# Kernel tuning notes

Hardware: AMD Instinct MI355X
Metric: run time of the kernel (lower is better)

## Reference

```python
import jax, jax.numpy as jnp
import numpy as np

N_HEADS = 8
N_LEVELS = 1
N_POINTS = 4
D_MODEL = 256
BATCH = 2
H0, W0 = 100, 150
LS = H0 * W0
LQ = 15000


def layer_norm(x, g, b, eps=1e-5):
    m = jnp.mean(x, -1, keepdims=True)
    v = jnp.var(x, -1, keepdims=True)
    return (x - m) * jax.lax.rsqrt(v + eps) * g + b


def bilinear_sample(v, Hl, Wl, loc):
    # v: [N, Hl*Wl, Hh, D] level features; loc in [0,1]: [N, Lq, Hh, P, 2] (x, y)
    Nb, _, Hh, D = v.shape
    Lq, P = loc.shape[1], loc.shape[3]
    x = loc[..., 0] * Wl - 0.5           # align_corners=False grid_sample convention
    y = loc[..., 1] * Hl - 0.5
    x0 = jnp.floor(x); y0 = jnp.floor(y)
    lx = (x - x0).transpose(0, 2, 1, 3)[..., None]   # [N,Hh,Lq,P,1]
    ly = (y - y0).transpose(0, 2, 1, 3)[..., None]
    x0i = x0.astype(jnp.int32); y0i = y0.astype(jnp.int32)
    vh = v.transpose(0, 2, 1, 3)                      # [N,Hh,Hl*Wl,D]

    def gather(xi, yi):
        valid = (xi >= 0) & (xi < Wl) & (yi >= 0) & (yi < Hl)   # zero padding
        idx = jnp.clip(yi, 0, Hl - 1) * Wl + jnp.clip(xi, 0, Wl - 1)
        idxf = idx.transpose(0, 2, 1, 3).reshape(Nb, Hh, Lq * P)
        g = jnp.take_along_axis(vh, idxf[..., None], axis=2).reshape(Nb, Hh, Lq, P, D)
        return g * valid.transpose(0, 2, 1, 3)[..., None]

    g00 = gather(x0i, y0i)
    g10 = gather(x0i + 1, y0i)
    g01 = gather(x0i, y0i + 1)
    g11 = gather(x0i + 1, y0i + 1)
    return (g00 * (1 - lx) * (1 - ly) + g10 * lx * (1 - ly)
            + g01 * (1 - lx) * ly + g11 * lx * ly)   # [N,Hh,Lq,P,D]


def ms_deform_attn(q, reference_points, src, shapes_np, starts_np, padding_mask,
                   W_val, b_val, W_off, b_off, W_attn, b_attn, W_out, b_out):
    Nb, Lq, C = q.shape
    Hh, D, L, P = N_HEADS, C // N_HEADS, N_LEVELS, N_POINTS
    value = src @ W_val + b_val
    value = jnp.where(padding_mask[..., None], 0.0, value).reshape(Nb, -1, Hh, D)
    offsets = (q @ W_off + b_off).reshape(Nb, Lq, Hh, L, P, 2)
    aw = jax.nn.softmax((q @ W_attn + b_attn).reshape(Nb, Lq, Hh, L * P), -1)
    aw = aw.reshape(Nb, Lq, Hh, L, P)
    # offset normalizer is (W, H) per level
    norm = jnp.asarray(shapes_np[:, ::-1].copy(), dtype=q.dtype)   # [L,2]
    loc = reference_points[:, :, None, :, None, :] + offsets / norm[None, None, None, :, None, :]
    out = 0.0
    for l in range(L):
        Hl, Wl = int(shapes_np[l, 0]), int(shapes_np[l, 1])
        s = int(starts_np[l])
        sampled = bilinear_sample(value[:, s:s + Hl * Wl], Hl, Wl, loc[:, :, :, l])
        out = out + jnp.sum(sampled * aw[:, :, :, l].transpose(0, 2, 1, 3)[..., None], axis=3)
    out = out.transpose(0, 2, 1, 3).reshape(Nb, Lq, C)
    return out @ W_out + b_out


def reference(tgt, query_pos, src_pos, tgt_spatial_shapes, reference_points,
              depth_reference_points, src, src_spatial_shapes, frame_start_index,
              src_padding_mask,
              W_dsa, b_dsa, g_nds, b_nds, W_off, b_off, W_attn, b_attn,
              W_val, b_val, W_out, b_out, W_csa, b_csa, g_n1, b_n1,
              W_ff, b_ff, g_n3, b_n3):
    ss = np.asarray(src_spatial_shapes)      # static level shapes
    starts = np.asarray(frame_start_index)
    # depth scale adaptation
    src_a = layer_norm(src @ W_dsa + b_dsa, g_nds, b_nds)
    q = tgt + query_pos
    tgt2 = ms_deform_attn(q, reference_points, src_a, ss, starts, src_padding_mask,
                          W_val, b_val, W_off, b_off, W_attn, b_attn, W_out, b_out)
    tgt2 = tgt2 @ W_csa + b_csa
    t = layer_norm(tgt + tgt2, g_n1, b_n1)
    # FFN: single linear d_model->d_model with exact GELU (per source code)
    ff = jax.nn.gelu(t @ W_ff + b_ff, approximate=False)
    return layer_norm(t + ff, g_n3, b_n3)


def setup_inputs() -> dict:
    key = jax.random.key(0)
    ks = jax.random.split(key, 24)
    C = D_MODEL
    Hh, L, P = N_HEADS, N_LEVELS, N_POINTS

    def lin(k, fin, fout, scale=None):
        s = (1.0 / np.sqrt(fin)) if scale is None else scale
        return (jax.random.normal(k, (fin, fout), jnp.float32) * s).astype(jnp.float32)

    inp = {}
    inp['tgt'] = jax.random.normal(ks[0], (BATCH, LQ, C), jnp.float32)
    inp['query_pos'] = 0.1 * jax.random.normal(ks[1], (BATCH, LQ, C), jnp.float32)
    inp['src_pos'] = 0.1 * jax.random.normal(ks[2], (BATCH, LS, C), jnp.float32)
    inp['tgt_spatial_shapes'] = jnp.array([[H0, W0]], jnp.int32)
    inp['reference_points'] = jax.random.uniform(ks[3], (BATCH, LQ, L, 2), jnp.float32)
    inp['depth_reference_points'] = jax.random.uniform(ks[4], (BATCH, LQ, 1, 2), jnp.float32)
    inp['src'] = jax.random.normal(ks[5], (BATCH, LS, C), jnp.float32)
    inp['src_spatial_shapes'] = jnp.array([[H0, W0]], jnp.int32)
    inp['frame_start_index'] = jnp.array([0], jnp.int32)
    inp['src_padding_mask'] = jnp.zeros((BATCH, LS), jnp.bool_)
    # parameters
    inp['W_dsa'] = lin(ks[6], C, C); inp['b_dsa'] = jnp.zeros((C,), jnp.float32)
    inp['g_nds'] = jnp.ones((C,), jnp.float32); inp['b_nds'] = jnp.zeros((C,), jnp.float32)
    inp['W_off'] = lin(ks[7], C, Hh * L * P * 2, scale=0.01)
    inp['b_off'] = 0.5 * jax.random.normal(ks[8], (Hh * L * P * 2,), jnp.float32)
    inp['W_attn'] = lin(ks[9], C, Hh * L * P)
    inp['b_attn'] = jnp.zeros((Hh * L * P,), jnp.float32)
    inp['W_val'] = lin(ks[10], C, C); inp['b_val'] = jnp.zeros((C,), jnp.float32)
    inp['W_out'] = lin(ks[11], C, C); inp['b_out'] = jnp.zeros((C,), jnp.float32)
    inp['W_csa'] = lin(ks[12], C, C); inp['b_csa'] = jnp.zeros((C,), jnp.float32)
    inp['g_n1'] = jnp.ones((C,), jnp.float32); inp['b_n1'] = jnp.zeros((C,), jnp.float32)
    inp['W_ff'] = lin(ks[13], C, C); inp['b_ff'] = jnp.zeros((C,), jnp.float32)
    inp['g_n3'] = jnp.ones((C,), jnp.float32); inp['b_n3'] = jnp.zeros((C,), jnp.float32)
    return inp
```

## Files before the change

### kernel.cpp

```cpp
#include <hip/hip_runtime.h>
#include <hip/hip_bf16.h>
#include <math.h>

#define LQ   15000
#define LS_  15000
#define NB   2
#define ROWS (NB*LQ)
#define HGT  100
#define WID  150

typedef __attribute__((ext_vector_type(8))) short bf16x8;
typedef __attribute__((ext_vector_type(4))) float f32x4;

__device__ inline short f2bf(float x) {
    __hip_bfloat16 h = __float2bfloat16(x);
    return *reinterpret_cast<short*>(&h);
}
__device__ inline unsigned pack2bf(float a, float b) {
    return ((unsigned)(unsigned short)f2bf(a)) | (((unsigned)(unsigned short)f2bf(b)) << 16);
}
__device__ inline float bf2f(short s) {
    return __uint_as_float(((unsigned)(unsigned short)s) << 16);
}
__device__ inline float gelu_exact(float x) {
    return 0.5f * x * (1.f + erff(x * 0.70710678118654752440f));
}

#if defined(__has_builtin)
#if __has_builtin(__builtin_amdgcn_global_load_lds)
#define HAS_GLL 1
#endif
#endif
#ifndef HAS_GLL
#define HAS_GLL 0
#endif

typedef unsigned int u32;

__device__ __forceinline__ void gld_lds16(const void* g, void* l) {
#if HAS_GLL
    __builtin_amdgcn_global_load_lds(
        (const __attribute__((address_space(1))) u32*)g,
        (__attribute__((address_space(3))) u32*)l,
        16, 0, 0);
#else
    int lane = threadIdx.x & 63;
    *(int4*)((char*)l + lane * 16) = *(const int4*)g;
#endif
}

template<int MODE>
__global__ __launch_bounds__(256, 2) void fused2(
    const void* __restrict__ Ap,
    const short* __restrict__ W1T, const float* __restrict__ bias1,
    const float* __restrict__ res1,
    const float* __restrict__ g1v, const float* __restrict__ b1v,
    const short* __restrict__ W2T, const float* __restrict__ bias2,
    void* __restrict__ Out,
    const unsigned char* __restrict__ mask,
    const float* __restrict__ g2v, const float* __restrict__ b2v,
    int M)
{
    __shared__ __align__(16) char lds[2 * 16384 + 64 * 264 * 2];
    short (*T)[264] = (short(*)[264])(lds + 32768);

    const int tid = threadIdx.x;
    const int bm0 = blockIdx.x * 64;
    const int wave = tid >> 6, lane = tid & 63;
    const int quad = lane >> 4, c = lane & 15;

    const int roff = c * 64 + ((quad ^ ((c >> 1) & 3)) << 4);

    auto stageB = [&](int buf, const short* __restrict__ W, int k0) {
        #pragma unroll
        for (int it = 0; it < 4; ++it) {
            int s = it * 256 + wave * 64 + lane;
            int n = s >> 2;
            int j = (s & 3) ^ ((n >> 1) & 3);
            gld_lds16(W + (size_t)n * 256 + k0 + j * 8,
                      lds + buf * 16384 + (it * 256 + wave * 64) * 16);
        }
    };

    int rA = bm0 + wave * 16 + c; if (rA > M - 1) rA = M - 1;
    bf16x8 aReg[8];

    stageB(0, W1T, 0);

    if (MODE == 1) {
        const short* A = (const short*)Ap + (size_t)rA * 256 + quad * 8;
        #pragma unroll
        for (int k = 0; k < 8; ++k) aReg[k] = *(const bf16x8*)(A + k * 32);
    } else {
        const float* A = (const float*)Ap + (size_t)rA * 256 + quad * 8;
        float4 lo[8], hi[8];
        #pragma unroll
        for (int k = 0; k < 8; ++k) {
            lo[k] = *(const float4*)(A + k * 32);
            hi[k] = *(const float4*)(A + k * 32 + 4);
        }
        #pragma unroll
        for (int k = 0; k < 8; ++k) {
            union { int4 i; bf16x8 v; } u;
            u.i.x = pack2bf(lo[k].x, lo[k].y);
            u.i.y = pack2bf(lo[k].z, lo[k].w);
            u.i.z = pack2bf(hi[k].x, hi[k].y);
            u.i.w = pack2bf(hi[k].z, hi[k].w);
            aReg[k] = u.v;
        }
    }

    f32x4 acc[16];
    #pragma unroll
    for (int t = 0; t < 16; ++t) acc[t] = (f32x4){0.f, 0.f, 0.f, 0.f};

    __syncthreads();

    #pragma unroll
    for (int k0c = 0; k0c < 8; ++k0c) {
        if (k0c < 7) stageB((k0c + 1) & 1, W1T, (k0c + 1) * 32);
        const char* bb = lds + (k0c & 1) * 16384 + roff;
        bf16x8 a = aReg[k0c];
        #pragma unroll
        for (int t = 0; t < 16; ++t) {
            bf16x8 b = *(const bf16x8*)(bb + t * 1024);
            acc[t] = __builtin_amdgcn_mfma_f32_16x16x32_bf16(a, b, acc[t], 0, 0, 0);
        }
        __syncthreads();
    }

    stageB(0, W2T, 0);

    {
        const int rb = wave * 16 + quad * 4;
        #pragma unroll
        for (int reg = 0; reg < 4; ++reg) {
            int rloc = rb + reg;
            int rg = bm0 + rloc; int rgl = (rg < M) ? rg : (M - 1);
            float s = 0.f, sq = 0.f;
            float vv[16];
            #pragma unroll
            for (int t = 0; t < 16; ++t) {
                int col = t * 16 + c;
                float v = acc[t][reg] + bias1[col];
                if (MODE == 1) v += res1[(size_t)rgl * 256 + col];
                vv[t] = v; s += v; sq += v * v;
            }
            #pragma unroll
            for (int o = 1; o < 16; o <<= 1) {
                s += __shfl_xor(s, o, 64); sq += __shfl_xor(sq, o, 64);
            }
            float mean = s * (1.f / 256.f);
            float var  = sq * (1.f / 256.f) - mean * mean;
            float rs   = rsqrtf(var + 1e-5f);
            #pragma unroll
            for (int t = 0; t < 16; ++t) {
                int col = t * 16 + c;
                T[rloc][col] = f2bf((vv[t] - mean) * rs * g1v[col] + b1v[col]);
            }
        }
    }

    #pragma unroll
    for (int k = 0; k < 8; ++k)
        aReg[k] = *(const bf16x8*)&T[wave * 16 + c][k * 32 + quad * 8];

    #pragma unroll
    for (int t = 0; t < 16; ++t) acc[t] = (f32x4){0.f, 0.f, 0.f, 0.f};

    __syncthreads();

    #pragma unroll
    for (int k0c = 0; k0c < 8; ++k0c) {
        if (k0c < 7) stageB((k0c + 1) & 1, W2T, (k0c + 1) * 32);
        const char* bb = lds + (k0c & 1) * 16384 + roff;
        bf16x8 a = aReg[k0c];
        #pragma unroll
        for (int t = 0; t < 16; ++t) {
            bf16x8 b = *(const bf16x8*)(bb + t * 1024);
            acc[t] = __builtin_amdgcn_mfma_f32_16x16x32_bf16(a, b, acc[t], 0, 0, 0);
        }
        __syncthreads();
    }

    const int rb = wave * 16 + quad * 4;
    if constexpr (MODE == 0) {
        short* O = (short*)Out;
        #pragma unroll
        for (int reg = 0; reg < 4; ++reg) {
            int rloc = rb + reg; int r = bm0 + rloc;
            if (r < M) {
                float mz = mask[r] ? 0.f : 1.f;
                int n = (r >= LS_) ? 1 : 0;
                int sidx = r - n * LS_;
                #pragma unroll
                for (int t = 0; t < 16; ++t) {
                    int col = t * 16 + c; int h = col >> 5, d = col & 31;
                    O[(((size_t)n * 8 + h) * LS_ + sidx) * 32 + d] =
                        f2bf((acc[t][reg] + bias2[col]) * mz);
                }
            }
        }
    } else {
        float* O = (float*)Out;
        #pragma unroll
        for (int reg = 0; reg < 4; ++reg) {
            int rloc = rb + reg; int r = bm0 + rloc;
            float s = 0.f, sq = 0.f;
            float vv[16];
            #pragma unroll
            for (int t = 0; t < 16; ++t) {
                int col = t * 16 + c;
                float v = gelu_exact(acc[t][reg] + bias2[col]) + bf2f(T[rloc][col]);
                vv[t] = v; s += v; sq += v * v;
            }
            #pragma unroll
            for (int o = 1; o < 16; o <<= 1) {
                s += __shfl_xor(s, o, 64); sq += __shfl_xor(sq, o, 64);
            }
            float mean = s * (1.f / 256.f);
            float var  = sq * (1.f / 256.f) - mean * mean;
            float rs   = rsqrtf(var + 1e-5f);
            if (r < M) {
                #pragma unroll
                for (int t = 0; t < 16; ++t) {
                    int col = t * 16 + c;
                    O[(size_t)r * 256 + col] = (vv[t] - mean) * rs * g2v[col] + b2v[col];
                }
            }
        }
    }
}

__global__ __launch_bounds__(256) void oa_gemm(
    const float* __restrict__ tgt, const float* __restrict__ qpos,
    const short* __restrict__ WToa, const float* __restrict__ b_oa,
    float* __restrict__ S_oa, int M)
{
    __shared__ short As[64][40];
    __shared__ short Bs[96][40];
    __shared__ float sb[96];

    const int tid = threadIdx.x;
    const int bm0 = blockIdx.x * 64;
    const int wave = tid >> 6, lane = tid & 63;
    const int quad = lane >> 4, c = lane & 15;

    if (tid < 96) sb[tid] = b_oa[tid];

    f32x4 acc[6];
    #pragma unroll
    for (int t = 0; t < 6; ++t) acc[t] = (f32x4){0.f, 0.f, 0.f, 0.f};

    for (int k0 = 0; k0 < 256; k0 += 32) {
        #pragma unroll
        for (int it = 0; it < 2; ++it) {
            int f = it * 256 + tid; int m = f >> 3; int ko = (f & 7) * 4;
            int r = bm0 + m; if (r > M - 1) r = M - 1;
            float4 v = *(const float4*)&tgt[(size_t)r * 256 + k0 + ko];
            float4 w = *(const float4*)&qpos[(size_t)r * 256 + k0 + ko];
            v.x += w.x; v.y += w.y; v.z += w.z; v.w += w.w;
            int2 p; p.x = pack2bf(v.x, v.y); p.y = pack2bf(v.z, v.w);
            *(int2*)&As[m][ko] = p;
        }
        {
            #pragma unroll
            for (int it = 0; it < 2; ++it) {
                int ff = it * 256 + tid;
                if (ff < 384) {
                    int n = ff >> 2; int ko = (ff & 3) * 8;
                    *(int4*)&Bs[n][ko] = *(const int4*)&WToa[(size_t)n * 256 + k0 + ko];
                }
            }
        }
        __syncthreads();
        bf16x8 a = *(const bf16x8*)&As[wave * 16 + c][quad * 8];
        #pragma unroll
        for (int t = 0; t < 6; ++t) {
            bf16x8 b = *(const bf16x8*)&Bs[t * 16 + c][quad * 8];
            acc[t] = __builtin_amdgcn_mfma_f32_16x16x32_bf16(a, b, acc[t], 0, 0, 0);
        }
        __syncthreads();
    }

    const int rb = wave * 16 + quad * 4;
    #pragma unroll
    for (int reg = 0; reg < 4; ++reg) {
        int r = bm0 + rb + reg;
        if (r < M) {
            #pragma unroll
            for (int t = 0; t < 6; ++t)
                S_oa[(size_t)r * 96 + t * 16 + c] = acc[t][reg] + sb[t * 16 + c];
        }
    }
}

__global__ __launch_bounds__(256) void deform_sample(
    const short* __restrict__ value,
    const float* __restrict__ S_oa,
    const float* __restrict__ refp,
    short* __restrict__ out)
{
    int grp = blockIdx.x * 32 + (threadIdx.x >> 3);
    int c4  = threadIdx.x & 7;
    int h = grp & 7;
    int r = grp >> 3;
    int n = (r >= LS_) ? 1 : 0;

    const float* row = S_oa + (size_t)r * 96;
    float rx = refp[(size_t)r * 2 + 0], ry = refp[(size_t)r * 2 + 1];
    float4 oA = *(const float4*)&row[h * 8];
    float4 oB = *(const float4*)&row[h * 8 + 4];
    float4 lg = *(const float4*)&row[64 + h * 4];

    float mx = fmaxf(fmaxf(lg.x, lg.y), fmaxf(lg.z, lg.w));
    float e0 = expf(lg.x - mx), e1 = expf(lg.y - mx), e2 = expf(lg.z - mx), e3 = expf(lg.w - mx);
    float inv = 1.f / (e0 + e1 + e2 + e3);
    float aw[4] = {e0 * inv, e1 * inv, e2 * inv, e3 * inv};
    float ox[4] = {oA.x, oA.z, oB.x, oB.z};
    float oy[4] = {oA.y, oA.w, oB.y, oB.w};

    const short* vb = value + (((size_t)n * 8 + h) * LS_) * 32 + c4 * 4;
    float a0 = 0.f, a1 = 0.f, a2 = 0.f, a3 = 0.f;

    #pragma unroll
    for (int p = 0; p < 4; ++p) {
        float x = rx * (float)WID + ox[p] - 0.5f;
        float y = ry * (float)HGT + oy[p] - 0.5f;
        float x0f = floorf(x), y0f = floorf(y);
        float lx = x - x0f, ly = y - y0f;
        int x0 = (int)x0f, y0 = (int)y0f;
        int x1 = x0 + 1, y1 = y0 + 1;
        bool vx0 = (x0 >= 0) & (x0 < WID), vx1 = (x1 >= 0) & (x1 < WID);
        bool vy0 = (y0 >= 0) & (y0 < HGT), vy1 = (y1 >= 0) & (y1 < HGT);
        float w00 = (vx0 & vy0) ? (1.f - lx) * (1.f - ly) * aw[p] : 0.f;
        float w10 = (vx1 & vy0) ? lx * (1.f - ly) * aw[p] : 0.f;
        float w01 = (vx0 & vy1) ? (1.f - lx) * ly * aw[p] : 0.f;
        float w11 = (vx1 & vy1) ? lx * ly * aw[p] : 0.f;
        int xc0 = min(max(x0, 0), WID - 1), xc1 = min(max(x1, 0), WID - 1);
        int yc0 = min(max(y0, 0), HGT - 1), yc1 = min(max(y1, 0), HGT - 1);
        int2 v00 = *(const int2*)&vb[(size_t)(yc0 * WID + xc0) * 32];
        int2 v10 = *(const int2*)&vb[(size_t)(yc0 * WID + xc1) * 32];
        int2 v01 = *(const int2*)&vb[(size_t)(yc1 * WID + xc0) * 32];
        int2 v11 = *(const int2*)&vb[(size_t)(yc1 * WID + xc1) * 32];
        a0 += w00 * __uint_as_float(((unsigned)v00.x) << 16)
            + w10 * __uint_as_float(((unsigned)v10.x) << 16)
            + w01 * __uint_as_float(((unsigned)v01.x) << 16)
            + w11 * __uint_as_float(((unsigned)v11.x) << 16);
        a1 += w00 * __uint_as_float(v00.x & 0xffff0000u)
            + w10 * __uint_as_float(v10.x & 0xffff0000u)
            + w01 * __uint_as_float(v01.x & 0xffff0000u)
            + w11 * __uint_as_float(v11.x & 0xffff0000u);
        a2 += w00 * __uint_as_float(((unsigned)v00.y) << 16)
            + w10 * __uint_as_float(((unsigned)v10.y) << 16)
            + w01 * __uint_as_float(((unsigned)v01.y) << 16)
            + w11 * __uint_as_float(((unsigned)v11.y) << 16);
        a3 += w00 * __uint_as_float(v00.y & 0xffff0000u)
            + w10 * __uint_as_float(v10.y & 0xffff0000u)
            + w01 * __uint_as_float(v01.y & 0xffff0000u)
            + w11 * __uint_as_float(v11.y & 0xffff0000u);
    }
    int2 o;
    o.x = pack2bf(a0, a1);
    o.y = pack2bf(a2, a3);
    *(int2*)&out[(size_t)r * 256 + h * 32 + c4 * 4] = o;
}

__global__ __launch_bounds__(256) void prep_all(
    const float* __restrict__ W_dsa, const float* __restrict__ W_val,
    const float* __restrict__ W_ff,  const float* __restrict__ W_out,
    const float* __restrict__ W_csa, const float* __restrict__ b_out,
    const float* __restrict__ b_csa, const float* __restrict__ W_off,
    const float* __restrict__ W_attn, const float* __restrict__ b_off,
    const float* __restrict__ b_attn,
    short* __restrict__ WT_dsa, short* __restrict__ WT_val, short* __restrict__ WT_ff,
    short* __restrict__ WT_c, float* __restrict__ bc,
    short* __restrict__ WT_oa, float* __restrict__ b_oa)
{
    __shared__ float tile[64][65];
    const int b = blockIdx.x, tid = threadIdx.x;
    if (b < 48) {
        const float* W = (b < 16) ? W_dsa : (b < 32) ? W_val : W_ff;
        short* WT = (b < 16) ? WT_dsa : (b < 32) ? WT_val : WT_ff;
        int t = b & 15; int bx = (t & 3) * 64, by = (t >> 2) * 64;
        #pragma unroll
        for (int it = 0; it < 4; ++it) {
            int f = it * 256 + tid; int i = f >> 4; int j = (f & 15) * 4;
            float4 v = *(const float4*)&W[(size_t)(by + i) * 256 + bx + j];
            tile[i][j] = v.x; tile[i][j + 1] = v.y; tile[i][j + 2] = v.z; tile[i][j + 3] = v.w;
        }
        __syncthreads();
        #pragma unroll
        for (int it = 0; it < 16; ++it) {
            int f = it * 256 + tid; int nl = f >> 6; int kl = f & 63;
            WT[(size_t)(bx + nl) * 256 + by + kl] = f2bf(tile[kl][nl]);
        }
    } else if (b < 304) {
        int k = b - 48, n = tid;
        float s = 0.f;
        #pragma unroll 8
        for (int j = 0; j < 256; ++j)
            s = fmaf(W_out[(size_t)k * 256 + j], W_csa[(size_t)j * 256 + n], s);
        WT_c[(size_t)n * 256 + k] = f2bf(s);
    } else if (b == 304) {
        int j = tid;
        float s = b_csa[j];
        #pragma unroll 8
        for (int k = 0; k < 256; ++k)
            s = fmaf(b_out[k], W_csa[(size_t)k * 256 + j], s);
        bc[j] = s;
    } else {
        int j = b - 305, k = tid;
        float v = (j < 64) ? W_off[(size_t)k * 64 + j] : W_attn[(size_t)k * 32 + (j - 64)];
        WT_oa[(size_t)j * 256 + k] = f2bf(v);
        if (k == 0) b_oa[j] = (j < 64) ? b_off[j] : b_attn[j - 64];
    }
}

extern "C" void kernel_launch(void* const* d_in, const int* in_sizes, int n_in,
                              void* d_out, int out_size, void* d_ws, size_t ws_size,
                              hipStream_t stream)
{
    const float* tgt       = (const float*)d_in[0];
    const float* query_pos = (const float*)d_in[1];
    const float* refp      = (const float*)d_in[4];
    const float* src       = (const float*)d_in[6];
    const unsigned char* mask = (const unsigned char*)d_in[9];
    const float* W_dsa  = (const float*)d_in[10]; const float* b_dsa  = (const float*)d_in[11];
    const float* g_nds  = (const float*)d_in[12]; const float* b_nds  = (const float*)d_in[13];
    const float* W_off  = (const float*)d_in[14]; const float* b_off  = (const float*)d_in[15];
    const float* W_attn = (const float*)d_in[16]; const float* b_attn = (const float*)d_in[17];
    const float* W_val  = (const float*)d_in[18]; const float* b_val  = (const float*)d_in[19];
    const float* W_out  = (const float*)d_in[20]; const float* b_out  = (const float*)d_in[21];
    const float* W_csa  = (const float*)d_in[22]; const float* b_csa  = (const float*)d_in[23];
    const float* g_n1   = (const float*)d_in[24]; const float* b_n1   = (const float*)d_in[25];
    const float* W_ff   = (const float*)d_in[26]; const float* b_ff   = (const float*)d_in[27];
    const float* g_n3   = (const float*)d_in[28]; const float* b_n3   = (const float*)d_in[29];
    float* out = (float*)d_out;

    short* attn_out = (short*)d_ws;
    short* value    = attn_out + (size_t)ROWS * 256;
    float* S_oa     = (float*)(value + (size_t)ROWS * 256);
    short* WT_dsa   = (short*)(S_oa + (size_t)ROWS * 96);
    short* WT_val   = WT_dsa + 65536;
    short* WT_ff    = WT_val + 65536;
    short* WT_c     = WT_ff + 65536;
    short* WT_oa    = WT_c + 65536;
    float* bc       = (float*)(WT_oa + 96 * 256);
    float* b_oa     = bc + 256;

    dim3 blk(256);
    const int GB = (ROWS + 63) / 64;

    prep_all<<<401, blk, 0, stream>>>(
        W_dsa, W_val, W_ff, W_out, W_csa, b_out, b_csa, W_off, W_attn, b_off, b_attn,
        WT_dsa, WT_val, WT_ff, WT_c, bc, WT_oa, b_oa);

    oa_gemm<<<GB, blk, 0, stream>>>(tgt, query_pos, WT_oa, b_oa, S_oa, ROWS);

    fused2<0><<<GB, blk, 0, stream>>>(
        src, WT_dsa, b_dsa, nullptr, g_nds, b_nds,
        WT_val, b_val, value, mask, nullptr, nullptr, ROWS);

    deform_sample<<<ROWS * 8 / 32, blk, 0, stream>>>(value, S_oa, refp, attn_out);

    fused2<1><<<GB, blk, 0, stream>>>(
        attn_out, WT_c, bc, tgt, g_n1, b_n1,
        WT_ff, b_ff, out, nullptr, g_n3, b_n3, ROWS);
}
```

Measured before the change: 293.7 us.

## Deepen weight prefetch pipeline in fused GEMM and restructure offset-attention GEMM

The fused two-GEMM kernel now prefetches two K-chunks of weights ahead, using explicit vmcnt waits and raw barriers instead of a full __syncthreads per step, so global-to-LDS loads overlap more with the MFMA work. In MODE 1 the LayerNorm residual is kept in fp32 registers instead of being re-read as bf16 from LDS, which raises register pressure and slightly changes the numerics. The offset/attention GEMM loads the whole weight matrix into LDS once and holds the summed tgt+qpos A rows in registers, which removes the per-K-step syncs. The hand-written waitcnt counts depend on the global_load_lds path issuing exactly four loads per stage.

```diff
diff --git a/kernel.cpp b/kernel.cpp
--- a/kernel.cpp
+++ b/kernel.cpp
@@ -48,6 +48,14 @@
     *(int4*)((char*)l + lane * 16) = *(const int4*)g;
 #endif
 }
+
+#if HAS_GLL
+#define WAIT_PREV() asm volatile("s_waitcnt vmcnt(4)" ::: "memory")
+#define WAIT_LAST() asm volatile("s_waitcnt vmcnt(0)" ::: "memory")
+#else
+#define WAIT_PREV() asm volatile("s_waitcnt vmcnt(0) lgkmcnt(0)" ::: "memory")
+#define WAIT_LAST() asm volatile("s_waitcnt vmcnt(0) lgkmcnt(0)" ::: "memory")
+#endif
 
 template<int MODE>
 __global__ __launch_bounds__(256, 2) void fused2(
@@ -85,8 +93,6 @@
     int rA = bm0 + wave * 16 + c; if (rA > M - 1) rA = M - 1;
     bf16x8 aReg[8];
 
-    stageB(0, W1T, 0);
-
     if (MODE == 1) {
         const short* A = (const short*)Ap + (size_t)rA * 256 + quad * 8;
         #pragma unroll
@@ -110,27 +116,33 @@
         }
     }
 
+    stageB(0, W1T, 0);
+    stageB(1, W1T, 32);
+
     f32x4 acc[16];
     #pragma unroll
     for (int t = 0; t < 16; ++t) acc[t] = (f32x4){0.f, 0.f, 0.f, 0.f};
 
-    __syncthreads();
-
-    #pragma unroll
-    for (int k0c = 0; k0c < 8; ++k0c) {
-        if (k0c < 7) stageB((k0c + 1) & 1, W1T, (k0c + 1) * 32);
-        const char* bb = lds + (k0c & 1) * 16384 + roff;
-        bf16x8 a = aReg[k0c];
+    #pragma unroll
+    for (int k = 0; k < 8; ++k) {
+        if (k < 7) { WAIT_PREV(); } else { WAIT_LAST(); }
+        __builtin_amdgcn_s_barrier();
+        const char* bb = lds + (k & 1) * 16384 + roff;
+        bf16x8 a = aReg[k];
         #pragma unroll
         for (int t = 0; t < 16; ++t) {
             bf16x8 b = *(const bf16x8*)(bb + t * 1024);
             acc[t] = __builtin_amdgcn_mfma_f32_16x16x32_bf16(a, b, acc[t], 0, 0, 0);
         }
-        __syncthreads();
+        asm volatile("" ::: "memory");
+        __builtin_amdgcn_s_barrier();
+        if (k < 6) stageB(k & 1, W1T, (k + 2) * 32);
     }
 
     stageB(0, W2T, 0);
-
+    stageB(1, W2T, 32);
+
+    float tres[4][16];
     {
         const int rb = wave * 16 + quad * 4;
         #pragma unroll
@@ -156,7 +168,9 @@
             #pragma unroll
             for (int t = 0; t < 16; ++t) {
                 int col = t * 16 + c;
-                T[rloc][col] = f2bf((vv[t] - mean) * rs * g1v[col] + b1v[col]);
+                float ln = (vv[t] - mean) * rs * g1v[col] + b1v[col];
+                if (MODE == 1) tres[reg][t] = ln;
+                T[rloc][col] = f2bf(ln);
             }
         }
     }
@@ -168,19 +182,20 @@
     #pragma unroll
     for (int t = 0; t < 16; ++t) acc[t] = (f32x4){0.f, 0.f, 0.f, 0.f};
 
-    __syncthreads();
-
-    #pragma unroll
-    for (int k0c = 0; k0c < 8; ++k0c) {
-        if (k0c < 7) stageB((k0c + 1) & 1, W2T, (k0c + 1) * 32);
-        const char* bb = lds + (k0c & 1) * 16384 + roff;
-        bf16x8 a = aReg[k0c];
+    #pragma unroll
+    for (int k = 0; k < 8; ++k) {
+        if (k < 7) { WAIT_PREV(); } else { WAIT_LAST(); }
+        __builtin_amdgcn_s_barrier();
+        const char* bb = lds + (k & 1) * 16384 + roff;
+        bf16x8 a = aReg[k];
         #pragma unroll
         for (int t = 0; t < 16; ++t) {
             bf16x8 b = *(const bf16x8*)(bb + t * 1024);
             acc[t] = __builtin_amdgcn_mfma_f32_16x16x32_bf16(a, b, acc[t], 0, 0, 0);
         }
-        __syncthreads();
+        asm volatile("" ::: "memory");
+        __builtin_amdgcn_s_barrier();
+        if (k < 6) stageB(k & 1, W2T, (k + 2) * 32);
     }
 
     const int rb = wave * 16 + quad * 4;
@@ -205,13 +220,13 @@
         float* O = (float*)Out;
         #pragma unroll
         for (int reg = 0; reg < 4; ++reg) {
-            int rloc = rb + reg; int r = bm0 + rloc;
+            int r = bm0 + rb + reg;
             float s = 0.f, sq = 0.f;
             float vv[16];
             #pragma unroll
             for (int t = 0; t < 16; ++t) {
                 int col = t * 16 + c;
-                float v = gelu_exact(acc[t][reg] + bias2[col]) + bf2f(T[rloc][col]);
+                float v = gelu_exact(acc[t][reg] + bias2[col]) + tres[reg][t];
                 vv[t] = v; s += v; sq += v * v;
             }
             #pragma unroll
@@ -237,8 +252,7 @@
     const short* __restrict__ WToa, const float* __restrict__ b_oa,
     float* __restrict__ S_oa, int M)
 {
-    __shared__ short As[64][40];
-    __shared__ short Bs[96][40];
+    __shared__ __align__(16) short Bs[96][264];
     __shared__ float sb[96];
 
     const int tid = threadIdx.x;
@@ -248,49 +262,55 @@
 
     if (tid < 96) sb[tid] = b_oa[tid];
 
+    #pragma unroll
+    for (int it = 0; it < 12; ++it) {
+        int f = it * 256 + tid;
+        int n = f >> 5, ko = (f & 31) * 8;
+        *(int4*)&Bs[n][ko] = *(const int4*)&WToa[(size_t)n * 256 + ko];
+    }
+
+    int r = bm0 + wave * 16 + c; if (r > M - 1) r = M - 1;
+    const float* At = tgt  + (size_t)r * 256 + quad * 8;
+    const float* Aq = qpos + (size_t)r * 256 + quad * 8;
+    bf16x8 aReg[8];
+    #pragma unroll
+    for (int k = 0; k < 8; ++k) {
+        float4 t0 = *(const float4*)(At + k * 32);
+        float4 t1 = *(const float4*)(At + k * 32 + 4);
+        float4 q0 = *(const float4*)(Aq + k * 32);
+        float4 q1 = *(const float4*)(Aq + k * 32 + 4);
+        union { int4 i; bf16x8 v; } u;
+        u.i.x = pack2bf(t0.x + q0.x, t0.y + q0.y);
+        u.i.y = pack2bf(t0.z + q0.z, t0.w + q0.w);
+        u.i.z = pack2bf(t1.x + q1.x, t1.y + q1.y);
+        u.i.w = pack2bf(t1.z + q1.z, t1.w + q1.w);
+        aReg[k] = u.v;
+    }
+
     f32x4 acc[6];
     #pragma unroll
     for (int t = 0; t < 6; ++t) acc[t] = (f32x4){0.f, 0.f, 0.f, 0.f};
 
-    for (int k0 = 0; k0 < 256; k0 += 32) {
-        #pragma unroll
-        for (int it = 0; it < 2; ++it) {
-            int f = it * 256 + tid; int m = f >> 3; int ko = (f & 7) * 4;
-            int r = bm0 + m; if (r > M - 1) r = M - 1;
-            float4 v = *(const float4*)&tgt[(size_t)r * 256 + k0 + ko];
-            float4 w = *(const float4*)&qpos[(size_t)r * 256 + k0 + ko];
-            v.x += w.x; v.y += w.y; v.z += w.z; v.w += w.w;
-            int2 p; p.x = pack2bf(v.x, v.y); p.y = pack2bf(v.z, v.w);
-            *(int2*)&As[m][ko] = p;
-        }
-        {
-            #pragma unroll
-            for (int it = 0; it < 2; ++it) {
-                int ff = it * 256 + tid;
-                if (ff < 384) {
-                    int n = ff >> 2; int ko = (ff & 3) * 8;
-                    *(int4*)&Bs[n][ko] = *(const int4*)&WToa[(size_t)n * 256 + k0 + ko];
-                }
-            }
-        }
-        __syncthreads();
-        bf16x8 a = *(const bf16x8*)&As[wave * 16 + c][quad * 8];
+    __syncthreads();
+
+    #pragma unroll
+    for (int k = 0; k < 8; ++k) {
+        bf16x8 a = aReg[k];
         #pragma unroll
         for (int t = 0; t < 6; ++t) {
-            bf16x8 b = *(const bf16x8*)&Bs[t * 16 + c][quad * 8];
+            bf16x8 b = *(const bf16x8*)&Bs[t * 16 + c][k * 32 + quad * 8];
             acc[t] = __builtin_amdgcn_mfma_f32_16x16x32_bf16(a, b, acc[t], 0, 0, 0);
         }
-        __syncthreads();
     }
 
     const int rb = wave * 16 + quad * 4;
     #pragma unroll
     for (int reg = 0; reg < 4; ++reg) {
-        int r = bm0 + rb + reg;
-        if (r < M) {
+        int rr = bm0 + rb + reg;
+        if (rr < M) {
             #pragma unroll
             for (int t = 0; t < 6; ++t)
-                S_oa[(size_t)r * 96 + t * 16 + c] = acc[t][reg] + sb[t * 16 + c];
+                S_oa[(size_t)rr * 96 + t * 16 + c] = acc[t][reg] + sb[t * 16 + c];
         }
     }
 }
```

New measurement: 298.1 us. Within noise of the previous version (+1.5%).
